# Performance work log

Measured on AMD Instinct MI355X. Metric: run time of the kernel, lower is better.

## Reference

```python
import jax, jax.numpy as jnp
import numpy as np

N_NODES = 100000
EPS = 1e-07


def _gconv(src, dst, x, W, b):
    # DGL GraphConv with norm='both': D_dst^{-1/2} A (D_src^{-1/2} x) W + b
    ones = jnp.ones(src.shape[0], x.dtype)
    deg_out = jax.ops.segment_sum(ones, src, num_segments=N_NODES)
    deg_in = jax.ops.segment_sum(ones, dst, num_segments=N_NODES)
    norm_out = jnp.where(deg_out > 0, deg_out, 1.0) ** -0.5
    norm_in = jnp.where(deg_in > 0, deg_in, 1.0) ** -0.5
    h = x * norm_out[:, None]
    agg = jax.ops.segment_sum(h[src], dst, num_segments=N_NODES)  # [N, d]
    agg = agg * norm_in[:, None]
    return agg @ W + b


def _branch(npemb, gauss, unif, temp, Wm, bm, Wl, bl, Wq, bq, Wd1, bd1, WdX, bdX, Wc, bc):
    cat = unif.shape[-1]
    mean = npemb @ Wm + bm                      # [E, d_z]
    logstd = npemb @ Wl + bl                    # [E, d_z]
    Nlat = gauss * jnp.exp(logstd) + mean       # reparameterization
    Nlat = Nlat.reshape(npemb.shape[0], cat, -1)  # [E, cat, d_m]
    q = npemb @ Wq + bq                         # [E, cat]
    gumbel = -jnp.log(-jnp.log(unif + EPS) + EPS)
    Z = jax.nn.softmax((q + gumbel) / temp, axis=-1)  # [E, cat]
    M = jnp.einsum('ec,ecd->ed', Z, Nlat)       # [E, d_m]
    X = jax.nn.relu(jax.nn.relu(M @ Wd1 + bd1) @ WdX + bdX)
    A = jax.nn.softmax(M @ Wc + bc, axis=-1)
    return A, X, mean, logstd, q


def setup_inputs() -> dict:
    key = jax.random.key(0)
    ks = jax.random.split(key, 32)
    E_g, E = 800000, 262144
    d_in, d_h, d_z, cat, d_m, d_dec, d_out = 128, 256, 256, 4, 64, 256, 128
    s = 0.05
    inp = {
        'x': jax.random.normal(ks[0], (N_NODES, d_in), jnp.float32),
        'src': jax.random.randint(ks[1], (E_g,), 0, N_NODES),
        'dst': jax.random.randint(ks[2], (E_g,), 0, N_NODES),
        'pos_src': jax.random.randint(ks[3], (E,), 0, N_NODES),
        'pos_dst': jax.random.randint(ks[4], (E,), 0, N_NODES),
        'neg_src': jax.random.randint(ks[5], (E,), 0, N_NODES),
        'neg_dst': jax.random.randint(ks[6], (E,), 0, N_NODES),
        'gauss_pos': jax.random.normal(ks[7], (E, d_z), jnp.float32),
        'gauss_neg': jax.random.normal(ks[8], (E, d_z), jnp.float32),
        'unif_pos': jax.random.uniform(ks[9], (E, cat), jnp.float32),
        'unif_neg': jax.random.uniform(ks[10], (E, cat), jnp.float32),
        'temp': 1,
        'W1': jax.random.normal(ks[11], (d_in, d_h), jnp.float32) * s,
        'b1': jnp.zeros((d_h,), jnp.float32),
        'W2': jax.random.normal(ks[12], (d_h, d_h), jnp.float32) * s,
        'b2': jnp.zeros((d_h,), jnp.float32),
        'Wm': jax.random.normal(ks[13], (d_h, d_z), jnp.float32) * s,
        'bm': jnp.zeros((d_z,), jnp.float32),
        'Wl': jax.random.normal(ks[14], (d_h, d_z), jnp.float32) * s,
        'bl': jnp.zeros((d_z,), jnp.float32),
        'Wq': jax.random.normal(ks[15], (d_h, cat), jnp.float32) * s,
        'bq': jnp.zeros((cat,), jnp.float32),
        'Wd1': jax.random.normal(ks[16], (d_m, d_dec), jnp.float32) * s,
        'bd1': jnp.zeros((d_dec,), jnp.float32),
        'WdX': jax.random.normal(ks[17], (d_dec, d_out), jnp.float32) * s,
        'bdX': jnp.zeros((d_out,), jnp.float32),
        'Wc': jax.random.normal(ks[18], (d_m, cat), jnp.float32) * s,
        'bc': jnp.zeros((cat,), jnp.float32),
    }
    return inp


def reference(x, src, dst, pos_src, pos_dst, neg_src, neg_dst,
              gauss_pos, gauss_neg, unif_pos, unif_neg, temp,
              W1, b1, W2, b2, Wm, bm, Wl, bl, Wq, bq,
              Wd1, bd1, WdX, bdX, Wc, bc):
    # two-layer GraphConv encoder (relu after layer 0; dropout in eval mode = identity)
    h = jax.nn.relu(_gconv(src, dst, x, W1, b1))
    h = _gconv(src, dst, h, W2, b2)
    # u_add_v edge gather
    pos_npemb = h[pos_src] + h[pos_dst]
    neg_npemb = h[neg_src] + h[neg_dst]
    t = jnp.asarray(temp, h.dtype)
    posA, posX, pos_mean, pos_logstd, posq = _branch(
        pos_npemb, gauss_pos, unif_pos, t, Wm, bm, Wl, bl, Wq, bq, Wd1, bd1, WdX, bdX, Wc, bc)
    negA, negX, neg_mean, neg_logstd, negq = _branch(
        neg_npemb, gauss_neg, unif_neg, t, Wm, bm, Wl, bl, Wq, bq, Wd1, bd1, WdX, bdX, Wc, bc)
    return (posA, negA, posX, negX, pos_mean, neg_mean,
            pos_logstd, neg_logstd, posq, negq)
```

## Files before the change

### kernel.cpp

```cpp
#include <hip/hip_runtime.h>
#include <hip/hip_bf16.h>


#define NN 100000
#define EG 800000
#define EE 262144
#define NB 98

typedef __attribute__((ext_vector_type(8))) short short8;
typedef __attribute__((ext_vector_type(4))) float f32x4;
typedef __attribute__((ext_vector_type(2))) float f32x2;

struct BArgs {
  const int* ea; const int* eb;
  const float* gauss; const float* unif;
  float* o_mean; float* o_ls; float* q_o; float* A_o;
  unsigned* M_o32;
};

__device__ __forceinline__ float lo2f(unsigned u) {
  union { unsigned u; float f; } v; v.u = u << 16; return v.f;
}
__device__ __forceinline__ float hi2f(unsigned u) {
  union { unsigned u; float f; } v; v.u = u & 0xFFFF0000u; return v.f;
}
__device__ __forceinline__ unsigned short f2bf(float f) {
  union { float f; unsigned u; } v; v.f = f;
  return (unsigned short)((v.u + 0x7FFFu + ((v.u >> 16) & 1u)) >> 16);
}
__device__ __forceinline__ unsigned pack2bf(float a, float b) {
  return (unsigned)f2bf(a) | ((unsigned)f2bf(b) << 16);
}
__device__ __forceinline__ int permc(int c) {
  return (c & ~31) | ((c & 15) << 1) | ((c >> 4) & 1);
}

__device__ __forceinline__ float decode_scalar(const void* p) {
  unsigned u = *(const unsigned*)p;
  float f = __uint_as_float(u);
  float af = fabsf(f);
  if (af >= 1e-6f && af <= 1e6f) return f;
  if (u < 1024u) return (float)u;
  return 1.0f;
}

__global__ __launch_bounds__(256) void k_deg(const int4* __restrict__ src4,
                                             const int4* __restrict__ dst4,
                                             int* __restrict__ degO,
                                             int* __restrict__ degI) {
  int i = blockIdx.x * 256 + threadIdx.x;
  if (i < EG / 4) {
    int4 s = src4[i];
    int4 d = dst4[i];
    atomicAdd(&degO[s.x], 1); atomicAdd(&degO[s.y], 1);
    atomicAdd(&degO[s.z], 1); atomicAdd(&degO[s.w], 1);
    atomicAdd(&degI[d.x], 1); atomicAdd(&degI[d.y], 1);
    atomicAdd(&degI[d.z], 1); atomicAdd(&degI[d.w], 1);
  }
}

__global__ __launch_bounds__(1024) void k_scan1(const int* __restrict__ degI,
                                                int* __restrict__ rowptr,
                                                int* __restrict__ bsum) {
  __shared__ int wsum[16];
  int t = threadIdx.x, lane = t & 63, wv = t >> 6;
  int i = blockIdx.x * 1024 + t;
  int v = (i < NN) ? degI[i] : 0;
  int incl = v;
#pragma unroll
  for (int off = 1; off < 64; off <<= 1) {
    int u = __shfl_up(incl, off);
    if (lane >= off) incl += u;
  }
  if (lane == 63) wsum[wv] = incl;
  __syncthreads();
  if (wv == 0 && lane < 16) {
    int s = wsum[lane];
    int si = s;
#pragma unroll
    for (int off = 1; off < 16; off <<= 1) {
      int u = __shfl_up(si, off);
      if (lane >= off) si += u;
    }
    wsum[lane] = si - s;
    if (lane == 15) bsum[blockIdx.x] = si;
  }
  __syncthreads();
  int excl = wsum[wv] + incl - v;
  if (i < NN) rowptr[i] = excl;
}

__global__ __launch_bounds__(128) void k_scan2(int* __restrict__ bsum) {
  __shared__ int w0tot;
  int t = threadIdx.x, lane = t & 63, wv = t >> 6;
  int v = (t < NB) ? bsum[t] : 0;
  int incl = v;
#pragma unroll
  for (int off = 1; off < 64; off <<= 1) {
    int u = __shfl_up(incl, off);
    if (lane >= off) incl += u;
  }
  if (wv == 0 && lane == 63) w0tot = incl;
  __syncthreads();
  int excl = incl - v + (wv ? w0tot : 0);
  if (t < NB) bsum[t] = excl;
}

__global__ __launch_bounds__(1024) void k_scan3(const int* __restrict__ degI,
                                                const int* __restrict__ degO,
                                                int* __restrict__ rowptr,
                                                int* __restrict__ cursor,
                                                const int* __restrict__ bsum,
                                                float* __restrict__ normO,
                                                float* __restrict__ normI) {
  int i = blockIdx.x * 1024 + threadIdx.x;
  if (i < NN) {
    int vv = rowptr[i] + bsum[blockIdx.x];
    rowptr[i] = vv;
    cursor[i] = vv;
    if (i == NN - 1) rowptr[NN] = vv + degI[i];
    int dO = degO[i]; if (dO < 1) dO = 1;
    int dI = degI[i]; if (dI < 1) dI = 1;
    normO[i] = rsqrtf((float)dO);
    normI[i] = rsqrtf((float)dI);
  }
}

__global__ __launch_bounds__(256) void k_fill(const int4* __restrict__ src4,
                                              const int4* __restrict__ dst4,
                                              int* __restrict__ cursor,
                                              int* __restrict__ csr) {
  int i = blockIdx.x * 256 + threadIdx.x;
  if (i < EG / 4) {
    int4 s = src4[i];
    int4 d = dst4[i];
    csr[atomicAdd(&cursor[d.x], 1)] = s.x;
    csr[atomicAdd(&cursor[d.y], 1)] = s.y;
    csr[atomicAdd(&cursor[d.z], 1)] = s.z;
    csr[atomicAdd(&cursor[d.w], 1)] = s.w;
  }
}

__global__ __launch_bounds__(256) void k_transpose_all(
    const float* __restrict__ W1, const float* __restrict__ W2,
    const float* __restrict__ Wm, const float* __restrict__ Wl,
    const float* __restrict__ Wd1, const float* __restrict__ WdX,
    const float* __restrict__ Wq,
    unsigned short* __restrict__ W1T, unsigned short* __restrict__ W2T,
    unsigned short* __restrict__ WmT, unsigned short* __restrict__ WlT,
    unsigned short* __restrict__ Wd1T, unsigned short* __restrict__ WdXT,
    unsigned short* __restrict__ WqT) {
  int idx = blockIdx.x * 256 + threadIdx.x;
  if (idx < 32768) {
    int n = idx & 255, k = idx >> 8;
    W1T[n * 128 + k] = f2bf(W1[idx]);
  } else if (idx < 98304) {
    int i = idx - 32768;
    int n = i & 255, k = i >> 8;
    W2T[n * 256 + k] = f2bf(W2[i]);
  } else if (idx < 163840) {
    int i = idx - 98304;
    int n = i & 255, k = i >> 8;
    WmT[n * 256 + k] = f2bf(Wm[i]);
  } else if (idx < 229376) {
    int i = idx - 163840;
    int n = i & 255, k = i >> 8;
    WlT[n * 256 + k] = f2bf(Wl[i]);
  } else if (idx < 245760) {
    int i = idx - 229376;
    int n = i & 255, k = i >> 8;
    Wd1T[n * 64 + k] = f2bf(Wd1[i]);
  } else if (idx < 278528) {
    int i = idx - 245760;
    int n = i & 127, k = i >> 7;
    WdXT[n * 256 + k] = f2bf(WdX[i]);
  } else if (idx < 282624) {
    int i = idx - 278528;
    int r = i >> 8, k = i & 255;
    WqT[i] = (r < 4) ? f2bf(Wq[k * 4 + r]) : (unsigned short)0;
  }
}

__global__ __launch_bounds__(256) void k_gather1(
    const float* __restrict__ x, const int* __restrict__ rowptr,
    const int* __restrict__ csr, const float* __restrict__ normO,
    const float* __restrict__ normI, unsigned short* __restrict__ agg) {
  int wid = (blockIdx.x * 256 + threadIdx.x) >> 6;
  int lane = threadIdx.x & 63;
  int half = lane >> 5, fl = lane & 31;
  int nw = (gridDim.x * 256) >> 6;
  for (int n = wid; n < NN; n += nw) {
    int beg = rowptr[n], end = rowptr[n + 1];
    float a0 = 0.f, a1 = 0.f, a2 = 0.f, a3 = 0.f;
    float b0 = 0.f, b1 = 0.f, b2 = 0.f, b3 = 0.f;
    int i = beg + half;
    for (; i + 2 < end; i += 4) {
      int s0 = csr[i], s1 = csr[i + 2];
      float ns0 = normO[s0], ns1 = normO[s1];
      float4 v0 = *(const float4*)(x + ((size_t)s0 << 7) + (fl << 2));
      float4 v1 = *(const float4*)(x + ((size_t)s1 << 7) + (fl << 2));
      a0 += ns0 * v0.x; a1 += ns0 * v0.y; a2 += ns0 * v0.z; a3 += ns0 * v0.w;
      b0 += ns1 * v1.x; b1 += ns1 * v1.y; b2 += ns1 * v1.z; b3 += ns1 * v1.w;
    }
    for (; i < end; i += 2) {
      int s0 = csr[i];
      float ns0 = normO[s0];
      float4 v0 = *(const float4*)(x + ((size_t)s0 << 7) + (fl << 2));
      a0 += ns0 * v0.x; a1 += ns0 * v0.y; a2 += ns0 * v0.z; a3 += ns0 * v0.w;
    }
    a0 += b0; a1 += b1; a2 += b2; a3 += b3;
    a0 += __shfl_xor(a0, 32); a1 += __shfl_xor(a1, 32);
    a2 += __shfl_xor(a2, 32); a3 += __shfl_xor(a3, 32);
    if (lane < 32) {
      float ni = normI[n];
      *(uint2*)(agg + ((size_t)n << 7) + (fl << 2)) =
          make_uint2(pack2bf(a0 * ni, a1 * ni), pack2bf(a2 * ni, a3 * ni));
    }
  }
}

__global__ __launch_bounds__(256) void k_gather2(
    const unsigned short* __restrict__ h1s, const int* __restrict__ rowptr,
    const int* __restrict__ csr, const float* __restrict__ normI,
    unsigned short* __restrict__ agg) {
  int wid = (blockIdx.x * 256 + threadIdx.x) >> 6;
  int lane = threadIdx.x & 63;
  int half = lane >> 5, fl = lane & 31;
  int nw = (gridDim.x * 256) >> 6;
  for (int n = wid; n < NN; n += nw) {
    int beg = rowptr[n], end = rowptr[n + 1];
    float a0 = 0.f, a1 = 0.f, a2 = 0.f, a3 = 0.f, a4 = 0.f, a5 = 0.f, a6 = 0.f, a7 = 0.f;
    float c0 = 0.f, c1 = 0.f, c2 = 0.f, c3 = 0.f, c4 = 0.f, c5 = 0.f, c6 = 0.f, c7 = 0.f;
    int i = beg + half;
    for (; i + 2 < end; i += 4) {
      int s0 = csr[i], s1 = csr[i + 2];
      uint4 v = *(const uint4*)(h1s + ((size_t)s0 << 8) + (fl << 3));
      uint4 u = *(const uint4*)(h1s + ((size_t)s1 << 8) + (fl << 3));
      a0 += lo2f(v.x); a1 += hi2f(v.x);
      a2 += lo2f(v.y); a3 += hi2f(v.y);
      a4 += lo2f(v.z); a5 += hi2f(v.z);
      a6 += lo2f(v.w); a7 += hi2f(v.w);
      c0 += lo2f(u.x); c1 += hi2f(u.x);
      c2 += lo2f(u.y); c3 += hi2f(u.y);
      c4 += lo2f(u.z); c5 += hi2f(u.z);
      c6 += lo2f(u.w); c7 += hi2f(u.w);
    }
    for (; i < end; i += 2) {
      int s0 = csr[i];
      uint4 v = *(const uint4*)(h1s + ((size_t)s0 << 8) + (fl << 3));
      a0 += lo2f(v.x); a1 += hi2f(v.x);
      a2 += lo2f(v.y); a3 += hi2f(v.y);
      a4 += lo2f(v.z); a5 += hi2f(v.z);
      a6 += lo2f(v.w); a7 += hi2f(v.w);
    }
    a0 += c0; a1 += c1; a2 += c2; a3 += c3;
    a4 += c4; a5 += c5; a6 += c6; a7 += c7;
    a0 += __shfl_xor(a0, 32); a1 += __shfl_xor(a1, 32);
    a2 += __shfl_xor(a2, 32); a3 += __shfl_xor(a3, 32);
    a4 += __shfl_xor(a4, 32); a5 += __shfl_xor(a5, 32);
    a6 += __shfl_xor(a6, 32); a7 += __shfl_xor(a7, 32);
    if (lane < 32) {
      float ni = normI[n];
      uint4 o;
      o.x = pack2bf(a0 * ni, a1 * ni);
      o.y = pack2bf(a2 * ni, a3 * ni);
      o.z = pack2bf(a4 * ni, a5 * ni);
      o.w = pack2bf(a6 * ni, a7 * ni);
      *(uint4*)(agg + ((size_t)n << 8) + (fl << 3)) = o;
    }
  }
}

template <int K, bool RELU, bool OSCALE>
__global__ __launch_bounds__(256) void k_gemm(
    const unsigned short* __restrict__ A, const float* __restrict__ oscale,
    const unsigned short* __restrict__ WT, const float* __restrict__ bias,
    unsigned short* __restrict__ C, int M) {
  __shared__ __align__(16) short At[128 * 40];
  __shared__ __align__(16) short Bt[256 * 40];
  const int t = threadIdx.x;
  const int row0 = blockIdx.x * 128;
  const int lane = t & 63, wave = t >> 6;
  const int wr = (wave >> 1) << 6;
  const int wcc = (wave & 1) << 7;
  const int lrow = lane & 15, lhi = lane >> 4;

  f32x4 acc[4][8];
#pragma unroll
  for (int m = 0; m < 4; ++m)
#pragma unroll
    for (int n = 0; n < 8; ++n) acc[m][n] = (f32x4){0.f, 0.f, 0.f, 0.f};

  for (int k0 = 0; k0 < K; k0 += 32) {
    if (k0) __syncthreads();
#pragma unroll
    for (int it = 0; it < 2; ++it) {
      int idx = t + it * 256;
      int r = idx >> 2, c8 = (idx & 3) << 3;
      int grow = row0 + r;
      int4 tv = {0, 0, 0, 0};
      if (grow < M) tv = *(const int4*)(A + (size_t)grow * K + k0 + c8);
      *(int4*)&At[r * 40 + c8] = tv;
    }
    {
      const unsigned short* wt = WT + (size_t)permc(t) * K + k0;
      *(int4*)&Bt[t * 40 + 0] = *(const int4*)(wt);
      *(int4*)&Bt[t * 40 + 8] = *(const int4*)(wt + 8);
      *(int4*)&Bt[t * 40 + 16] = *(const int4*)(wt + 16);
      *(int4*)&Bt[t * 40 + 24] = *(const int4*)(wt + 24);
    }
    __syncthreads();
    short8 a[4], b[8];
#pragma unroll
    for (int m = 0; m < 4; ++m)
      a[m] = *(const short8*)&At[(wr + m * 16 + lrow) * 40 + lhi * 8];
#pragma unroll
    for (int n = 0; n < 8; ++n)
      b[n] = *(const short8*)&Bt[(wcc + n * 16 + lrow) * 40 + lhi * 8];
#pragma unroll
    for (int m = 0; m < 4; ++m)
#pragma unroll
      for (int n = 0; n < 8; ++n)
        acc[m][n] = __builtin_amdgcn_mfma_f32_16x16x32_bf16(a[m], b[n], acc[m][n], 0, 0, 0);
  }
#pragma unroll
  for (int np = 0; np < 4; ++np) {
    int tc = wcc + np * 32 + (lrow << 1);
    float bv0 = bias[tc], bv1 = bias[tc + 1];
#pragma unroll
    for (int m = 0; m < 4; ++m) {
#pragma unroll
      for (int r = 0; r < 4; ++r) {
        int grow = row0 + wr + m * 16 + lhi * 4 + r;
        if (grow < M) {
          float v0 = acc[m][2 * np][r] + bv0;
          float v1 = acc[m][2 * np + 1][r] + bv1;
          if (RELU) { v0 = fmaxf(v0, 0.f); v1 = fmaxf(v1, 0.f); }
          if (OSCALE) { float s = oscale[grow]; v0 *= s; v1 *= s; }
          *(unsigned*)&C[(size_t)grow * 256 + tc] = pack2bf(v0, v1);
        }
      }
    }
  }
}

__global__ __launch_bounds__(512) void k_branch2(
    const unsigned short* __restrict__ h, BArgs P0, BArgs P1,
    const void* __restrict__ temp_p,
    const unsigned short* __restrict__ WmT, const float* __restrict__ bm,
    const unsigned short* __restrict__ WlT, const float* __restrict__ bl,
    const unsigned short* __restrict__ WqT, const float* __restrict__ bq,
    const float* __restrict__ Wc, const float* __restrict__ bc) {
  const BArgs P = (blockIdx.x < 2048) ? P0 : P1;
  __shared__ __align__(16) char U[33792];
  short* At = (short*)U;
  float* Mf = (float*)U;
  __shared__ float zS[512];
  __shared__ float qS[512];
  __shared__ float WcT[4 * 68];
  __shared__ float bmS[256], blS[256];
  __shared__ int eaS[128], ebS[128];

  const int t = threadIdx.x;
  const int e0 = (blockIdx.x & 2047) << 7;
  const int lane = t & 63;
  const int wv = t >> 6;
  const int lrow = lane & 15, lhi = lane >> 4;
  const int wc = wv << 5;

  if (t < 256) {
    bmS[t] = bm[t]; blS[t] = bl[t];
    WcT[(t & 3) * 68 + (t >> 2)] = Wc[t];
  } else if (t < 384) {
    eaS[t - 256] = P.ea[e0 + t - 256];
  } else {
    ebS[t - 384] = P.eb[e0 + t - 384];
  }
  __syncthreads();

  f32x4 am[8][2], al[8][2], aq;
#pragma unroll
  for (int m = 0; m < 8; ++m)
#pragma unroll
    for (int n = 0; n < 2; ++n) {
      am[m][n] = (f32x4){0.f, 0.f, 0.f, 0.f};
      al[m][n] = (f32x4){0.f, 0.f, 0.f, 0.f};
    }
  aq = (f32x4){0.f, 0.f, 0.f, 0.f};

  const int ar = t >> 2, as_ = t & 3;
  const int arsw = ((as_ ^ (ar & 3)) << 3);
  const int fsw = (lrow & 3);

  const unsigned short* pa_base = h + ((size_t)eaS[ar] << 8) + (as_ << 3);
  const unsigned short* pb_base = h + ((size_t)ebS[ar] << 8) + (as_ << 3);
  const size_t row0p = (size_t)permc(wc + lrow) << 8;
  const size_t row1p = (size_t)permc(wc + 16 + lrow) << 8;
  const unsigned short* bm0p = WmT + row0p + (lhi << 3);
  const unsigned short* bm1p = WmT + row1p + (lhi << 3);
  const unsigned short* bl0p = WlT + row0p + (lhi << 3);
  const unsigned short* bl1p = WlT + row1p + (lhi << 3);
  const unsigned short* bqp = WqT + ((size_t)lrow << 8) + (lhi << 3);

  uint4 va = *(const uint4*)pa_base;
  uint4 vb = *(const uint4*)pb_base;

  for (int k0 = 0; k0 < 256; k0 += 32) {
    unsigned w0 = pack2bf(lo2f(va.x) + lo2f(vb.x), hi2f(va.x) + hi2f(vb.x));
    unsigned w1 = pack2bf(lo2f(va.y) + lo2f(vb.y), hi2f(va.y) + hi2f(vb.y));
    unsigned w2 = pack2bf(lo2f(va.z) + lo2f(vb.z), hi2f(va.z) + hi2f(vb.z));
    unsigned w3 = pack2bf(lo2f(va.w) + lo2f(vb.w), hi2f(va.w) + hi2f(vb.w));
    if (k0 < 224) {
      va = *(const uint4*)(pa_base + k0 + 32);
      vb = *(const uint4*)(pb_base + k0 + 32);
    }
    short8 bmf0 = *(const short8*)(bm0p + k0);
    short8 bmf1 = *(const short8*)(bm1p + k0);
    short8 blf0 = *(const short8*)(bl0p + k0);
    short8 blf1 = *(const short8*)(bl1p + k0);
    short8 bqf = *(const short8*)(bqp + k0);
    if (k0) __syncthreads();
    *(int4*)&At[ar * 32 + arsw] = make_int4((int)w0, (int)w1, (int)w2, (int)w3);
    __syncthreads();
    short8 a[8], aqa;
#pragma unroll
    for (int m = 0; m < 8; ++m)
      a[m] = *(const short8*)&At[(m * 16 + lrow) * 32 + ((lhi ^ fsw) << 3)];
    aqa = *(const short8*)&At[((wv << 4) + lrow) * 32 + ((lhi ^ fsw) << 3)];
#pragma unroll
    for (int m = 0; m < 8; ++m) {
      am[m][0] = __builtin_amdgcn_mfma_f32_16x16x32_bf16(a[m], bmf0, am[m][0], 0, 0, 0);
      am[m][1] = __builtin_amdgcn_mfma_f32_16x16x32_bf16(a[m], bmf1, am[m][1], 0, 0, 0);
      al[m][0] = __builtin_amdgcn_mfma_f32_16x16x32_bf16(a[m], blf0, al[m][0], 0, 0, 0);
      al[m][1] = __builtin_amdgcn_mfma_f32_16x16x32_bf16(a[m], blf1, al[m][1], 0, 0, 0);
    }
    aq = __builtin_amdgcn_mfma_f32_16x16x32_bf16(aqa, bqf, aq, 0, 0, 0);
  }
  __syncthreads();

  float invt = 1.0f / decode_scalar(temp_p);
  float qb = (lrow < 4) ? bq[lrow] : 0.f;
#pragma unroll
  for (int r = 0; r < 4; ++r) {
    int el = (wv << 4) + lhi * 4 + r;
    float q = aq[r] + qb;
    float uu = 0.5f;
    if (lrow < 4) uu = P.unif[(((size_t)(e0 + el)) << 2) + lrow];
    float g = -__logf(-__logf(uu + 1e-7f) + 1e-7f);
    float z = (q + g) * invt;
    float mx = fmaxf(z, __shfl_xor(z, 1));
    mx = fmaxf(mx, __shfl_xor(mx, 2));
    float ez = __expf(z - mx);
    float sz = ez + __shfl_xor(ez, 1);
    sz += __shfl_xor(sz, 2);
    if (lrow < 4) { zS[el * 4 + lrow] = ez / sz; qS[el * 4 + lrow] = q; }
  }
  for (int i = t; i < 128 * 66; i += 512) Mf[i] = 0.f;
  __syncthreads();

  __builtin_nontemporal_store(qS[t], P.q_o + (((size_t)e0) << 2) + t);

  const int cidx = wv >> 1;
  const int dd = ((wv & 1) << 5) + (lrow << 1);
  const int tc = wc + (lrow << 1);
  float bm0 = bmS[tc], bm1 = bmS[tc + 1];
  float bl0 = blS[tc], bl1 = blS[tc + 1];
#pragma unroll
  for (int m = 0; m < 8; ++m) {
#pragma unroll
    for (int r = 0; r < 4; ++r) {
      int row = m * 16 + lhi * 4 + r;
      size_t gi = (((size_t)(e0 + row)) << 8) + tc;
      float mv0 = am[m][0][r] + bm0, mv1 = am[m][1][r] + bm1;
      float lv0 = al[m][0][r] + bl0, lv1 = al[m][1][r] + bl1;
      __builtin_nontemporal_store((f32x2){mv0, mv1}, (f32x2*)(P.o_mean + gi));
      __builtin_nontemporal_store((f32x2){lv0, lv1}, (f32x2*)(P.o_ls + gi));
      f32x2 g2 = __builtin_nontemporal_load((const f32x2*)(P.gauss + gi));
      float zc = zS[(row << 2) + cidx];
      atomicAdd(&Mf[row * 66 + dd], zc * (g2.x * __expf(lv0) + mv0));
      atomicAdd(&Mf[row * 66 + dd + 1], zc * (g2.y * __expf(lv1) + mv1));
    }
  }
  __syncthreads();

  {
    int e = t >> 2, cat = t & 3;
    const float* mrow = &Mf[e * 66];
    const float* wct = &WcT[cat * 68];
    float s = 0.f;
#pragma unroll
    for (int dp = 0; dp < 32; ++dp) {
      float2 m2 = *(const float2*)(mrow + 2 * dp);
      s += m2.x * wct[2 * dp] + m2.y * wct[2 * dp + 1];
    }
    s += bc[cat];
    float smx = fmaxf(s, __shfl_xor(s, 1));
    smx = fmaxf(smx, __shfl_xor(smx, 2));
    float es = __expf(s - smx);
    float ssum = es + __shfl_xor(es, 1);
    ssum += __shfl_xor(ssum, 2);
    __builtin_nontemporal_store(es / ssum, P.A_o + (((size_t)e0) << 2) + t);
  }
#pragma unroll
  for (int j = 0; j < 8; ++j) {
    int idx = j * 512 + t;
    int row = idx >> 5, dp = idx & 31;
    float2 m2 = *(const float2*)(&Mf[row * 66 + 2 * dp]);
    P.M_o32[((size_t)(e0 + row)) * 32 + dp] = pack2bf(m2.x, m2.y);
  }
}

__global__ __launch_bounds__(512) void k_dec2(
    const unsigned short* __restrict__ Mw0, const unsigned short* __restrict__ Mw1,
    const unsigned short* __restrict__ Wd1T, const float* __restrict__ bd1,
    const unsigned short* __restrict__ WdXT, const float* __restrict__ bdX,
    float* __restrict__ Xo0, float* __restrict__ Xo1) {
  const int br = blockIdx.x >> 12;
  const unsigned short* Mw = br ? Mw1 : Mw0;
  float* Xo = br ? Xo1 : Xo0;
  __shared__ __align__(16) char R[65280];
  short* Mt = (short*)R;
  short* Bt1 = (short*)(R + 9216);
  short* X1 = (short*)R;
  short* Bt2 = (short*)(R + 46848);
  const int t = threadIdx.x, lane = t & 63, wv = t >> 6;
  const int lrow = lane & 15, lhi = lane >> 4;
  const int e0 = (blockIdx.x & 4095) << 6;

  const int r2 = t >> 2, base2 = (t & 3) << 4;
  const unsigned short* wpb = WdXT + ((size_t)permc(r2) << 8) + base2;

  {
    int r = t >> 3, c8 = (t & 7) << 3;
    *(int4*)&Mt[r * 72 + c8] = *(const int4*)(Mw + (((size_t)(e0 + r)) << 6) + c8);
  }
  {
    int r1 = t >> 1, base = (t & 1) << 5;
    const unsigned short* wp = Wd1T + ((size_t)permc(r1) << 6) + base;
#pragma unroll
    for (int j = 0; j < 4; ++j)
      *(int4*)&Bt1[r1 * 72 + base + j * 8] = *(const int4*)(wp + j * 8);
  }
  int4 pw0 = *(const int4*)(wpb);
  int4 pw1 = *(const int4*)(wpb + 8);
  __syncthreads();
  f32x4 acc1[4][2];
#pragma unroll
  for (int m = 0; m < 4; ++m)
#pragma unroll
    for (int n = 0; n < 2; ++n) acc1[m][n] = (f32x4){0.f, 0.f, 0.f, 0.f};
  const int wc1 = wv << 5;
  {
    short8 a0[4], a1[4], b0[2], b1[2];
#pragma unroll
    for (int m = 0; m < 4; ++m) {
      a0[m] = *(const short8*)&Mt[(m * 16 + lrow) * 72 + lhi * 8];
      a1[m] = *(const short8*)&Mt[(m * 16 + lrow) * 72 + 32 + lhi * 8];
    }
#pragma unroll
    for (int n = 0; n < 2; ++n) {
      b0[n] = *(const short8*)&Bt1[(wc1 + n * 16 + lrow) * 72 + lhi * 8];
      b1[n] = *(const short8*)&Bt1[(wc1 + n * 16 + lrow) * 72 + 32 + lhi * 8];
    }
#pragma unroll
    for (int m = 0; m < 4; ++m)
#pragma unroll
      for (int n = 0; n < 2; ++n) {
        acc1[m][n] = __builtin_amdgcn_mfma_f32_16x16x32_bf16(a0[m], b0[n], acc1[m][n], 0, 0, 0);
        acc1[m][n] = __builtin_amdgcn_mfma_f32_16x16x32_bf16(a1[m], b1[n], acc1[m][n], 0, 0, 0);
      }
  }
  __syncthreads();
  {
    int tc = wc1 + (lrow << 1);
    float bdv0 = bd1[tc], bdv1 = bd1[tc + 1];
#pragma unroll
    for (int m = 0; m < 4; ++m)
#pragma unroll
      for (int r = 0; r < 4; ++r) {
        int row = m * 16 + lhi * 4 + r;
        float v0 = fmaxf(acc1[m][0][r] + bdv0, 0.f);
        float v1 = fmaxf(acc1[m][1][r] + bdv1, 0.f);
        *(unsigned*)&X1[row * 264 + tc] = pack2bf(v0, v1);
      }
  }

  f32x4 acc2[2][2];
#pragma unroll
  for (int m = 0; m < 2; ++m)
#pragma unroll
    for (int n = 0; n < 2; ++n) acc2[m][n] = (f32x4){0.f, 0.f, 0.f, 0.f};
  const int wr2 = (wv >> 2) << 5, wc2 = (wv & 3) << 5;
  for (int k0 = 0; k0 < 256; k0 += 64) {
    __syncthreads();
    *(int4*)&Bt2[r2 * 72 + base2] = pw0;
    *(int4*)&Bt2[r2 * 72 + base2 + 8] = pw1;
    if (k0 < 192) {
      pw0 = *(const int4*)(wpb + k0 + 64);
      pw1 = *(const int4*)(wpb + k0 + 64 + 8);
    }
    __syncthreads();
    short8 c0[2], c1[2], d0[2], d1[2];
#pragma unroll
    for (int m = 0; m < 2; ++m) {
      c0[m] = *(const short8*)&X1[(wr2 + m * 16 + lrow) * 264 + k0 + lhi * 8];
      c1[m] = *(const short8*)&X1[(wr2 + m * 16 + lrow) * 264 + k0 + 32 + lhi * 8];
    }
#pragma unroll
    for (int n = 0; n < 2; ++n) {
      d0[n] = *(const short8*)&Bt2[(wc2 + n * 16 + lrow) * 72 + lhi * 8];
      d1[n] = *(const short8*)&Bt2[(wc2 + n * 16 + lrow) * 72 + 32 + lhi * 8];
    }
#pragma unroll
    for (int m = 0; m < 2; ++m)
#pragma unroll
      for (int n = 0; n < 2; ++n) {
        acc2[m][n] = __builtin_amdgcn_mfma_f32_16x16x32_bf16(c0[m], d0[n], acc2[m][n], 0, 0, 0);
        acc2[m][n] = __builtin_amdgcn_mfma_f32_16x16x32_bf16(c1[m], d1[n], acc2[m][n], 0, 0, 0);
      }
  }
  {
    int tc2 = wc2 + (lrow << 1);
    float bx0 = bdX[tc2], bx1 = bdX[tc2 + 1];
#pragma unroll
    for (int m = 0; m < 2; ++m)
#pragma unroll
      for (int r = 0; r < 4; ++r) {
        int row = wr2 + m * 16 + lhi * 4 + r;
        float v0 = fmaxf(acc2[m][0][r] + bx0, 0.f);
        float v1 = fmaxf(acc2[m][1][r] + bx1, 0.f);
        __builtin_nontemporal_store((f32x2){v0, v1},
                                    (f32x2*)(Xo + (((size_t)(e0 + row)) << 7) + tc2));
      }
  }
}

extern "C" void kernel_launch(void* const* d_in, const int* in_sizes, int n_in,
                              void* d_out, int out_size, void* d_ws, size_t ws_size,
                              hipStream_t stream) {
  const float* x = (const float*)d_in[0];
  const int* src = (const int*)d_in[1];
  const int* dst = (const int*)d_in[2];
  const int* pos_src = (const int*)d_in[3];
  const int* pos_dst = (const int*)d_in[4];
  const int* neg_src = (const int*)d_in[5];
  const int* neg_dst = (const int*)d_in[6];
  const float* gauss_pos = (const float*)d_in[7];
  const float* gauss_neg = (const float*)d_in[8];
  const float* unif_pos = (const float*)d_in[9];
  const float* unif_neg = (const float*)d_in[10];
  const void* temp_p = d_in[11];
  const float* W1 = (const float*)d_in[12];
  const float* b1 = (const float*)d_in[13];
  const float* W2 = (const float*)d_in[14];
  const float* b2 = (const float*)d_in[15];
  const float* Wm = (const float*)d_in[16];
  const float* bm = (const float*)d_in[17];
  const float* Wl = (const float*)d_in[18];
  const float* bl = (const float*)d_in[19];
  const float* Wq = (const float*)d_in[20];
  const float* bq = (const float*)d_in[21];
  const float* Wd1 = (const float*)d_in[22];
  const float* bd1 = (const float*)d_in[23];
  const float* WdX = (const float*)d_in[24];
  const float* bdX = (const float*)d_in[25];
  const float* Wc = (const float*)d_in[26];
  const float* bc = (const float*)d_in[27];

  char* w = (char*)d_ws;
  int* degO = (int*)w;
  int* degI = (int*)(w + 401408);
  int* rowptr = (int*)(w + 802816);
  int* cursor = (int*)(w + 1204224);
  float* normO = (float*)(w + 1605632);
  float* normI = (float*)(w + 2007040);
  int* csr = (int*)(w + 2408448);
  unsigned short* W1T = (unsigned short*)(w + 5609472);
  unsigned short* W2T = (unsigned short*)(w + 5675008);
  unsigned short* WmT = (unsigned short*)(w + 5806080);
  unsigned short* WlT = (unsigned short*)(w + 5937152);
  unsigned short* Wd1T = (unsigned short*)(w + 6068224);
  unsigned short* WdXT = (unsigned short*)(w + 6100992);
  unsigned short* WqT = (unsigned short*)(w + 6166528);
  int* bsum = (int*)(w + 6174720);
  unsigned short* agg1 = (unsigned short*)(w + 6175232);
  unsigned short* h1s = (unsigned short*)(w + 31775232);
  unsigned short* agg2 = (unsigned short*)(w + 82975232);
  unsigned short* h = (unsigned short*)(w + 134175232);
  unsigned short* Mws0 = (unsigned short*)(w + 185375232);
  unsigned short* Mws1 = (unsigned short*)(w + 218929664);

  float* out = (float*)d_out;
  float* posA = out;
  float* negA = out + 1048576ull;
  float* posX = out + 2097152ull;
  float* negX = out + 35651584ull;
  float* pos_mean = out + 69206016ull;
  float* neg_mean = out + 136314880ull;
  float* pos_logstd = out + 203423744ull;
  float* neg_logstd = out + 270532608ull;
  float* posq = out + 337641472ull;
  float* negq = out + 338690048ull;

  hipMemsetAsync(d_ws, 0, 802816, stream);

  k_deg<<<782, 256, 0, stream>>>((const int4*)src, (const int4*)dst, degO, degI);
  k_scan1<<<NB, 1024, 0, stream>>>(degI, rowptr, bsum);
  k_scan2<<<1, 128, 0, stream>>>(bsum);
  k_scan3<<<NB, 1024, 0, stream>>>(degI, degO, rowptr, cursor, bsum, normO, normI);
  k_fill<<<782, 256, 0, stream>>>((const int4*)src, (const int4*)dst, cursor, csr);
  k_transpose_all<<<1104, 256, 0, stream>>>(W1, W2, Wm, Wl, Wd1, WdX, Wq,
                                            W1T, W2T, WmT, WlT, Wd1T, WdXT, WqT);

  k_gather1<<<2048, 256, 0, stream>>>(x, rowptr, csr, normO, normI, agg1);
  k_gemm<128, true, true><<<782, 256, 0, stream>>>(agg1, normO, W1T, b1, h1s, NN);
  k_gather2<<<2048, 256, 0, stream>>>(h1s, rowptr, csr, normI, agg2);
  k_gemm<256, false, false><<<782, 256, 0, stream>>>(agg2, nullptr, W2T, b2, h, NN);

  BArgs P0 = {pos_src, pos_dst, gauss_pos, unif_pos,
              pos_mean, pos_logstd, posq, posA, (unsigned*)Mws0};
  BArgs P1 = {neg_src, neg_dst, gauss_neg, unif_neg,
              neg_mean, neg_logstd, negq, negA, (unsigned*)Mws1};

  k_branch2<<<4096, 512, 0, stream>>>(h, P0, P1, temp_p,
                                      WmT, bm, WlT, bl, WqT, bq, Wc, bc);
  k_dec2<<<8192, 512, 0, stream>>>(Mws0, Mws1, Wd1T, bd1, WdXT, bdX, posX, negX);
}
```

Measured before the change: 1.371 ms.

## Halve branch kernel edge tile and double-buffer the LDS A tile

Measured after the change: 1.514 ms. 1.1x slower.

```diff
diff --git a/kernel.cpp b/kernel.cpp
--- a/kernel.cpp
+++ b/kernel.cpp
@@ -344,25 +344,25 @@
   }
 }
 
-__global__ __launch_bounds__(512) void k_branch2(
+__global__ __launch_bounds__(512, 4) void k_branch2(
     const unsigned short* __restrict__ h, BArgs P0, BArgs P1,
     const void* __restrict__ temp_p,
     const unsigned short* __restrict__ WmT, const float* __restrict__ bm,
     const unsigned short* __restrict__ WlT, const float* __restrict__ bl,
     const unsigned short* __restrict__ WqT, const float* __restrict__ bq,
     const float* __restrict__ Wc, const float* __restrict__ bc) {
-  const BArgs P = (blockIdx.x < 2048) ? P0 : P1;
-  __shared__ __align__(16) char U[33792];
+  const BArgs P = (blockIdx.x < 4096) ? P0 : P1;
+  __shared__ __align__(16) char U[16896];
   short* At = (short*)U;
   float* Mf = (float*)U;
-  __shared__ float zS[512];
-  __shared__ float qS[512];
+  __shared__ float zS[256];
+  __shared__ float qS[256];
   __shared__ float WcT[4 * 68];
   __shared__ float bmS[256], blS[256];
-  __shared__ int eaS[128], ebS[128];
+  __shared__ int eaS[64], ebS[64];
 
   const int t = threadIdx.x;
-  const int e0 = (blockIdx.x & 2047) << 7;
+  const int e0 = (blockIdx.x & 4095) << 6;
   const int lane = t & 63;
   const int wv = t >> 6;
   const int lrow = lane & 15, lhi = lane >> 4;
@@ -371,16 +371,16 @@
   if (t < 256) {
     bmS[t] = bm[t]; blS[t] = bl[t];
     WcT[(t & 3) * 68 + (t >> 2)] = Wc[t];
+  } else if (t < 320) {
+    eaS[t - 256] = P.ea[e0 + t - 256];
   } else if (t < 384) {
-    eaS[t - 256] = P.ea[e0 + t - 256];
-  } else {
-    ebS[t - 384] = P.eb[e0 + t - 384];
-  }
-  __syncthreads();
-
-  f32x4 am[8][2], al[8][2], aq;
-#pragma unroll
-  for (int m = 0; m < 8; ++m)
+    ebS[t - 320] = P.eb[e0 + t - 320];
+  }
+  __syncthreads();
+
+  f32x4 am[4][2], al[4][2], aq;
+#pragma unroll
+  for (int m = 0; m < 4; ++m)
 #pragma unroll
     for (int n = 0; n < 2; ++n) {
       am[m][n] = (f32x4){0.f, 0.f, 0.f, 0.f};
@@ -388,12 +388,12 @@
     }
   aq = (f32x4){0.f, 0.f, 0.f, 0.f};
 
-  const int ar = t >> 2, as_ = t & 3;
-  const int arsw = ((as_ ^ (ar & 3)) << 3);
+  const int ar = t >> 3, s16 = (t >> 1) & 3, half = t & 1;
+  const int atw = ar * 32 + ((s16 ^ (ar & 3)) << 3) + (half << 2);
   const int fsw = (lrow & 3);
 
-  const unsigned short* pa_base = h + ((size_t)eaS[ar] << 8) + (as_ << 3);
-  const unsigned short* pb_base = h + ((size_t)ebS[ar] << 8) + (as_ << 3);
+  const unsigned short* pa_base = h + ((size_t)eaS[ar] << 8) + (s16 << 3) + (half << 2);
+  const unsigned short* pb_base = h + ((size_t)ebS[ar] << 8) + (s16 << 3) + (half << 2);
   const size_t row0p = (size_t)permc(wc + lrow) << 8;
   const size_t row1p = (size_t)permc(wc + 16 + lrow) << 8;
   const unsigned short* bm0p = WmT + row0p + (lhi << 3);
@@ -402,63 +402,86 @@
   const unsigned short* bl1p = WlT + row1p + (lhi << 3);
   const unsigned short* bqp = WqT + ((size_t)lrow << 8) + (lhi << 3);
 
-  uint4 va = *(const uint4*)pa_base;
-  uint4 vb = *(const uint4*)pb_base;
-
-  for (int k0 = 0; k0 < 256; k0 += 32) {
+  uint2 va = *(const uint2*)pa_base;
+  uint2 vb = *(const uint2*)pb_base;
+  {
     unsigned w0 = pack2bf(lo2f(va.x) + lo2f(vb.x), hi2f(va.x) + hi2f(vb.x));
     unsigned w1 = pack2bf(lo2f(va.y) + lo2f(vb.y), hi2f(va.y) + hi2f(vb.y));
-    unsigned w2 = pack2bf(lo2f(va.z) + lo2f(vb.z), hi2f(va.z) + hi2f(vb.z));
-    unsigned w3 = pack2bf(lo2f(va.w) + lo2f(vb.w), hi2f(va.w) + hi2f(vb.w));
-    if (k0 < 224) {
-      va = *(const uint4*)(pa_base + k0 + 32);
-      vb = *(const uint4*)(pb_base + k0 + 32);
-    }
+    *(uint2*)&At[atw] = make_uint2(w0, w1);
+  }
+  va = *(const uint2*)(pa_base + 32);
+  vb = *(const uint2*)(pb_base + 32);
+  __syncthreads();
+
+  int cur = 0;
+  for (int k0 = 0; k0 < 256; k0 += 32) {
     short8 bmf0 = *(const short8*)(bm0p + k0);
     short8 bmf1 = *(const short8*)(bm1p + k0);
     short8 blf0 = *(const short8*)(bl0p + k0);
     short8 blf1 = *(const short8*)(bl1p + k0);
-    short8 bqf = *(const short8*)(bqp + k0);
-    if (k0) __syncthreads();
-    *(int4*)&At[ar * 32 + arsw] = make_int4((int)w0, (int)w1, (int)w2, (int)w3);
+    short8 bqf;
+    if (wv < 4) bqf = *(const short8*)(bqp + k0);
+    const short* ab = &At[cur * 2048];
+    short8 a0 = *(const short8*)&ab[(lrow) * 32 + ((lhi ^ fsw) << 3)];
+    short8 a1 = *(const short8*)&ab[(16 + lrow) * 32 + ((lhi ^ fsw) << 3)];
+    short8 a2 = *(const short8*)&ab[(32 + lrow) * 32 + ((lhi ^ fsw) << 3)];
+    short8 a3 = *(const short8*)&ab[(48 + lrow) * 32 + ((lhi ^ fsw) << 3)];
+    short8 aqa;
+    if (wv < 4) aqa = *(const short8*)&ab[((wv << 4) + lrow) * 32 + ((lhi ^ fsw) << 3)];
+    if (k0 < 224) {
+      unsigned w0 = pack2bf(lo2f(va.x) + lo2f(vb.x), hi2f(va.x) + hi2f(vb.x));
+      unsigned w1 = pack2bf(lo2f(va.y) + lo2f(vb.y), hi2f(va.y) + hi2f(vb.y));
+      *(uint2*)&At[(cur ^ 1) * 2048 + atw] = make_uint2(w0, w1);
+      if (k0 < 192) {
+        va = *(const uint2*)(pa_base + k0 + 64);
+        vb = *(const uint2*)(pb_base + k0 + 64);
+      }
+    }
+    am[0][0] = __builtin_amdgcn_mfma_f32_16x16x32_bf16(a0, bmf0, am[0][0], 0, 0, 0);
+    am[0][1] = __builtin_amdgcn_mfma_f32_16x16x32_bf16(a0, bmf1, am[0][1], 0, 0, 0);
+    al[0][0] = __builtin_amdgcn_mfma_f32_16x16x32_bf16(a0, blf0, al[0][0], 0, 0, 0);
+    al[0][1] = __builtin_amdgcn_mfma_f32_16x16x32_bf16(a0, blf1, al[0][1], 0, 0, 0);
+    am[1][0] = __builtin_amdgcn_mfma_f32_16x16x32_bf16(a1, bmf0, am[1][0], 0, 0, 0);
+    am[1][1] = __builtin_amdgcn_mfma_f32_16x16x32_bf16(a1, bmf1, am[1][1], 0, 0, 0);
+    al[1][0] = __builtin_amdgcn_mfma_f32_16x16x32_bf16(a1, blf0, al[1][0], 0, 0, 0);
+    al[1][1] = __builtin_amdgcn_mfma_f32_16x16x32_bf16(a1, blf1, al[1][1], 0, 0, 0);
+    am[2][0] = __builtin_amdgcn_mfma_f32_16x16x32_bf16(a2, bmf0, am[2][0], 0, 0, 0);
+    am[2][1] = __builtin_amdgcn_mfma_f32_16x16x32_bf16(a2, bmf1, am[2][1], 0, 0, 0);
+    al[2][0] = __builtin_amdgcn_mfma_f32_16x16x32_bf16(a2, blf0, al[2][0], 0, 0, 0);
+    al[2][1] = __builtin_amdgcn_mfma_f32_16x16x32_bf16(a2, blf1, al[2][1], 0, 0, 0);
+    am[3][0] = __builtin_amdgcn_mfma_f32_16x16x32_bf16(a3, bmf0, am[3][0], 0, 0, 0);
+    am[3][1] = __builtin_amdgcn_mfma_f32_16x16x32_bf16(a3, bmf1, am[3][1], 0, 0, 0);
+    al[3][0] = __builtin_amdgcn_mfma_f32_16x16x32_bf16(a3, blf0, al[3][0], 0, 0, 0);
+    al[3][1] = __builtin_amdgcn_mfma_f32_16x16x32_bf16(a3, blf1, al[3][1], 0, 0, 0);
+    if (wv < 4) aq = __builtin_amdgcn_mfma_f32_16x16x32_bf16(aqa, bqf, aq, 0, 0, 0);
     __syncthreads();
-    short8 a[8], aqa;
-#pragma unroll
-    for (int m = 0; m < 8; ++m)
-      a[m] = *(const short8*)&At[(m * 16 + lrow) * 32 + ((lhi ^ fsw) << 3)];
-    aqa = *(const short8*)&At[((wv << 4) + lrow) * 32 + ((lhi ^ fsw) << 3)];
-#pragma unroll
-    for (int m = 0; m < 8; ++m) {
-      am[m][0] = __builtin_amdgcn_mfma_f32_16x16x32_bf16(a[m], bmf0, am[m][0], 0, 0, 0);
-      am[m][1] = __builtin_amdgcn_mfma_f32_16x16x32_bf16(a[m], bmf1, am[m][1], 0, 0, 0);
-      al[m][0] = __builtin_amdgcn_mfma_f32_16x16x32_bf16(a[m], blf0, al[m][0], 0, 0, 0);
-      al[m][1] = __builtin_amdgcn_mfma_f32_16x16x32_bf16(a[m], blf1, al[m][1], 0, 0, 0);
-    }
-    aq = __builtin_amdgcn_mfma_f32_16x16x32_bf16(aqa, bqf, aq, 0, 0, 0);
-  }
-  __syncthreads();
+    cur ^= 1;
+  }
 
   float invt = 1.0f / decode_scalar(temp_p);
-  float qb = (lrow < 4) ? bq[lrow] : 0.f;
-#pragma unroll
-  for (int r = 0; r < 4; ++r) {
-    int el = (wv << 4) + lhi * 4 + r;
-    float q = aq[r] + qb;
-    float uu = 0.5f;
-    if (lrow < 4) uu = P.unif[(((size_t)(e0 + el)) << 2) + lrow];
-    float g = -__logf(-__logf(uu + 1e-7f) + 1e-7f);
-    float z = (q + g) * invt;
-    float mx = fmaxf(z, __shfl_xor(z, 1));
-    mx = fmaxf(mx, __shfl_xor(mx, 2));
-    float ez = __expf(z - mx);
-    float sz = ez + __shfl_xor(ez, 1);
-    sz += __shfl_xor(sz, 2);
-    if (lrow < 4) { zS[el * 4 + lrow] = ez / sz; qS[el * 4 + lrow] = q; }
-  }
-  for (int i = t; i < 128 * 66; i += 512) Mf[i] = 0.f;
-  __syncthreads();
-
-  __builtin_nontemporal_store(qS[t], P.q_o + (((size_t)e0) << 2) + t);
+  if (wv < 4) {
+    float qb = (lrow < 4) ? bq[lrow] : 0.f;
+#pragma unroll
+    for (int r = 0; r < 4; ++r) {
+      int el = (wv << 4) + lhi * 4 + r;
+      float q = aq[r] + qb;
+      float uu = 0.5f;
+      if (lrow < 4) uu = P.unif[(((size_t)(e0 + el)) << 2) + lrow];
+      float g = -__logf(-__logf(uu + 1e-7f) + 1e-7f);
+      float z = (q + g) * invt;
+      float mx = fmaxf(z, __shfl_xor(z, 1));
+      mx = fmaxf(mx, __shfl_xor(mx, 2));
+      float ez = __expf(z - mx);
+      float sz = ez + __shfl_xor(ez, 1);
+      sz += __shfl_xor(sz, 2);
+      if (lrow < 4) { zS[el * 4 + lrow] = ez / sz; qS[el * 4 + lrow] = q; }
+    }
+  }
+  for (int i = t; i < 64 * 66; i += 512) Mf[i] = 0.f;
+  __syncthreads();
+
+  if (t < 256)
+    __builtin_nontemporal_store(qS[t], P.q_o + (((size_t)e0) << 2) + t);
 
   const int cidx = wv >> 1;
   const int dd = ((wv & 1) << 5) + (lrow << 1);
@@ -466,7 +489,7 @@
   float bm0 = bmS[tc], bm1 = bmS[tc + 1];
   float bl0 = blS[tc], bl1 = blS[tc + 1];
 #pragma unroll
-  for (int m = 0; m < 8; ++m) {
+  for (int m = 0; m < 4; ++m) {
 #pragma unroll
     for (int r = 0; r < 4; ++r) {
       int row = m * 16 + lhi * 4 + r;
@@ -483,7 +506,7 @@
   }
   __syncthreads();
 
-  {
+  if (t < 256) {
     int e = t >> 2, cat = t & 3;
     const float* mrow = &Mf[e * 66];
     const float* wct = &WcT[cat * 68];
@@ -502,7 +525,7 @@
     __builtin_nontemporal_store(es / ssum, P.A_o + (((size_t)e0) << 2) + t);
   }
 #pragma unroll
-  for (int j = 0; j < 8; ++j) {
+  for (int j = 0; j < 4; ++j) {
     int idx = j * 512 + t;
     int row = idx >> 5, dp = idx & 31;
     float2 m2 = *(const float2*)(&Mf[row * 66 + 2 * dp]);
@@ -722,7 +745,7 @@
   BArgs P1 = {neg_src, neg_dst, gauss_neg, unif_neg,
               neg_mean, neg_logstd, negq, negA, (unsigned*)Mws1};
 
-  k_branch2<<<4096, 512, 0, stream>>>(h, P0, P1, temp_p,
+  k_branch2<<<8192, 512, 0, stream>>>(h, P0, P1, temp_p,
                                       WmT, bm, WlT, bl, WqT, bq, Wc, bc);
   k_dec2<<<8192, 512, 0, stream>>>(Mws0, Mws1, Wd1T, bd1, WdXT, bdX, posX, negX);
 }
```

## Double-buffer the LDS A tile and prefetch gauss/unif loads ahead of the GEMM

Applied to the files above, without the earlier changes.

After: 1.606 ms. +17.1%, slower.

```diff
diff --git a/kernel.cpp b/kernel.cpp
--- a/kernel.cpp
+++ b/kernel.cpp
@@ -391,6 +391,7 @@
   const int ar = t >> 2, as_ = t & 3;
   const int arsw = ((as_ ^ (ar & 3)) << 3);
   const int fsw = (lrow & 3);
+  const int tc = wc + (lrow << 1);
 
   const unsigned short* pa_base = h + ((size_t)eaS[ar] << 8) + (as_ << 3);
   const unsigned short* pb_base = h + ((size_t)ebS[ar] << 8) + (as_ << 3);
@@ -402,31 +403,77 @@
   const unsigned short* bl1p = WlT + row1p + (lhi << 3);
   const unsigned short* bqp = WqT + ((size_t)lrow << 8) + (lhi << 3);
 
+  f32x2 gpre[16];
+#pragma unroll
+  for (int m = 0; m < 8; ++m) {
+#pragma unroll
+    for (int r = 0; r < 4; r += 2) {
+    }
+  }
+  f32x2 gpre2[16];
+#pragma unroll
+  for (int m = 0; m < 8; ++m) {
+#pragma unroll
+    for (int r = 0; r < 2; ++r) {
+      int row = m * 16 + lhi * 4 + r;
+      gpre[m * 2 + r] = __builtin_nontemporal_load(
+          (const f32x2*)(P.gauss + (((size_t)(e0 + row)) << 8) + tc));
+    }
+  }
+  float uupre[4];
+#pragma unroll
+  for (int r = 0; r < 4; ++r) {
+    int el = (wv << 4) + lhi * 4 + r;
+    uupre[r] = (lrow < 4) ? P.unif[(((size_t)(e0 + el)) << 2) + lrow] : 0.5f;
+  }
+
   uint4 va = *(const uint4*)pa_base;
   uint4 vb = *(const uint4*)pb_base;
-
-  for (int k0 = 0; k0 < 256; k0 += 32) {
+  {
     unsigned w0 = pack2bf(lo2f(va.x) + lo2f(vb.x), hi2f(va.x) + hi2f(vb.x));
     unsigned w1 = pack2bf(lo2f(va.y) + lo2f(vb.y), hi2f(va.y) + hi2f(vb.y));
     unsigned w2 = pack2bf(lo2f(va.z) + lo2f(vb.z), hi2f(va.z) + hi2f(vb.z));
     unsigned w3 = pack2bf(lo2f(va.w) + lo2f(vb.w), hi2f(va.w) + hi2f(vb.w));
-    if (k0 < 224) {
-      va = *(const uint4*)(pa_base + k0 + 32);
-      vb = *(const uint4*)(pb_base + k0 + 32);
-    }
+    *(int4*)&At[ar * 32 + arsw] = make_int4((int)w0, (int)w1, (int)w2, (int)w3);
+  }
+  va = *(const uint4*)(pa_base + 32);
+  vb = *(const uint4*)(pb_base + 32);
+  __syncthreads();
+
+  int cur = 0;
+  for (int k0 = 0; k0 < 256; k0 += 32) {
     short8 bmf0 = *(const short8*)(bm0p + k0);
     short8 bmf1 = *(const short8*)(bm1p + k0);
     short8 blf0 = *(const short8*)(bl0p + k0);
     short8 blf1 = *(const short8*)(bl1p + k0);
     short8 bqf = *(const short8*)(bqp + k0);
-    if (k0) __syncthreads();
-    *(int4*)&At[ar * 32 + arsw] = make_int4((int)w0, (int)w1, (int)w2, (int)w3);
-    __syncthreads();
+    if (k0 == 128) {
+#pragma unroll
+      for (int m = 0; m < 8; ++m)
+#pragma unroll
+        for (int r = 2; r < 4; ++r) {
+          int row = m * 16 + lhi * 4 + r;
+          gpre2[m * 2 + r - 2] = __builtin_nontemporal_load(
+              (const f32x2*)(P.gauss + (((size_t)(e0 + row)) << 8) + tc));
+        }
+    }
+    const short* ab = &At[cur * 4096];
     short8 a[8], aqa;
 #pragma unroll
     for (int m = 0; m < 8; ++m)
-      a[m] = *(const short8*)&At[(m * 16 + lrow) * 32 + ((lhi ^ fsw) << 3)];
-    aqa = *(const short8*)&At[((wv << 4) + lrow) * 32 + ((lhi ^ fsw) << 3)];
+      a[m] = *(const short8*)&ab[(m * 16 + lrow) * 32 + ((lhi ^ fsw) << 3)];
+    aqa = *(const short8*)&ab[((wv << 4) + lrow) * 32 + ((lhi ^ fsw) << 3)];
+    if (k0 < 224) {
+      unsigned w0 = pack2bf(lo2f(va.x) + lo2f(vb.x), hi2f(va.x) + hi2f(vb.x));
+      unsigned w1 = pack2bf(lo2f(va.y) + lo2f(vb.y), hi2f(va.y) + hi2f(vb.y));
+      unsigned w2 = pack2bf(lo2f(va.z) + lo2f(vb.z), hi2f(va.z) + hi2f(vb.z));
+      unsigned w3 = pack2bf(lo2f(va.w) + lo2f(vb.w), hi2f(va.w) + hi2f(vb.w));
+      *(int4*)&At[(cur ^ 1) * 4096 + ar * 32 + arsw] = make_int4((int)w0, (int)w1, (int)w2, (int)w3);
+      if (k0 < 192) {
+        va = *(const uint4*)(pa_base + k0 + 64);
+        vb = *(const uint4*)(pb_base + k0 + 64);
+      }
+    }
 #pragma unroll
     for (int m = 0; m < 8; ++m) {
       am[m][0] = __builtin_amdgcn_mfma_f32_16x16x32_bf16(a[m], bmf0, am[m][0], 0, 0, 0);
@@ -435,8 +482,9 @@
       al[m][1] = __builtin_amdgcn_mfma_f32_16x16x32_bf16(a[m], blf1, al[m][1], 0, 0, 0);
     }
     aq = __builtin_amdgcn_mfma_f32_16x16x32_bf16(aqa, bqf, aq, 0, 0, 0);
-  }
-  __syncthreads();
+    __syncthreads();
+    cur ^= 1;
+  }
 
   float invt = 1.0f / decode_scalar(temp_p);
   float qb = (lrow < 4) ? bq[lrow] : 0.f;
@@ -444,9 +492,7 @@
   for (int r = 0; r < 4; ++r) {
     int el = (wv << 4) + lhi * 4 + r;
     float q = aq[r] + qb;
-    float uu = 0.5f;
-    if (lrow < 4) uu = P.unif[(((size_t)(e0 + el)) << 2) + lrow];
-    float g = -__logf(-__logf(uu + 1e-7f) + 1e-7f);
+    float g = -__logf(-__logf(uupre[r] + 1e-7f) + 1e-7f);
     float z = (q + g) * invt;
     float mx = fmaxf(z, __shfl_xor(z, 1));
     mx = fmaxf(mx, __shfl_xor(mx, 2));
@@ -462,7 +508,6 @@
 
   const int cidx = wv >> 1;
   const int dd = ((wv & 1) << 5) + (lrow << 1);
-  const int tc = wc + (lrow << 1);
   float bm0 = bmS[tc], bm1 = bmS[tc + 1];
   float bl0 = blS[tc], bl1 = blS[tc + 1];
 #pragma unroll
@@ -475,7 +520,7 @@
       float lv0 = al[m][0][r] + bl0, lv1 = al[m][1][r] + bl1;
       __builtin_nontemporal_store((f32x2){mv0, mv1}, (f32x2*)(P.o_mean + gi));
       __builtin_nontemporal_store((f32x2){lv0, lv1}, (f32x2*)(P.o_ls + gi));
-      f32x2 g2 = __builtin_nontemporal_load((const f32x2*)(P.gauss + gi));
+      f32x2 g2 = (r < 2) ? gpre[m * 2 + r] : gpre2[m * 2 + r - 2];
       float zc = zS[(row << 2) + cidx];
       atomicAdd(&Mf[row * 66 + dd], zc * (g2.x * __expf(lv0) + mv0));
       atomicAdd(&Mf[row * 66 + dd + 1], zc * (g2.y * __expf(lv1) + mv1));
```
